# Performance work log

Measured on AMD Instinct MI355X. Metric: run time of the kernel, lower is better.

## Reference

```python
import jax, jax.numpy as jnp
import numpy as np

N_EMBD = 1024
N_HEAD = 16
HEAD_SIZE = 64
EPS = 1e-5


def _layer_norm(x, gamma, beta, eps=EPS):
    mu = jnp.mean(x, axis=-1, keepdims=True)
    var = jnp.mean(jnp.square(x - mu), axis=-1, keepdims=True)
    return (x - mu) * jax.lax.rsqrt(var + eps) * gamma + beta


def setup_inputs() -> dict:
    key = jax.random.key(0)
    ks = jax.random.split(key, 10)
    C = N_EMBD
    s = 1.0 / np.sqrt(C)
    x = jax.random.normal(ks[0], (4, 2048, C), dtype=jnp.float32)
    Wq = jax.random.normal(ks[1], (C, C), dtype=jnp.float32) * s
    Wk = jax.random.normal(ks[2], (C, C), dtype=jnp.float32) * s
    Wv = jax.random.normal(ks[3], (C, C), dtype=jnp.float32) * s
    Wo = jax.random.normal(ks[4], (C, C), dtype=jnp.float32) * s
    W1 = jax.random.normal(ks[5], (C, 4 * C), dtype=jnp.float32) * s
    b1 = jnp.zeros((4 * C,), dtype=jnp.float32)
    W2 = jax.random.normal(ks[6], (4 * C, C), dtype=jnp.float32) * (1.0 / np.sqrt(4 * C))
    b2 = jnp.zeros((C,), dtype=jnp.float32)
    g1 = jnp.ones((C,), dtype=jnp.float32)
    be1 = jnp.zeros((C,), dtype=jnp.float32)
    g2 = jnp.ones((C,), dtype=jnp.float32)
    be2 = jnp.zeros((C,), dtype=jnp.float32)
    return {"x": x, "Wq": Wq, "Wk": Wk, "Wv": Wv, "Wo": Wo,
            "W1": W1, "b1": b1, "W2": W2, "b2": b2,
            "g1": g1, "be1": be1, "g2": g2, "be2": be2}


def _block(x, Wq, Wk, Wv, Wo, W1, b1, W2, b2, g1, be1, g2, be2):
    B, T, C = x.shape
    H, D = N_HEAD, HEAD_SIZE
    # attention sub-block
    h = _layer_norm(x, g1, be1)
    q = (h @ Wq.T).reshape(B, T, H, D).transpose(0, 2, 1, 3)  # [B,H,T,D]
    k = (h @ Wk.T).reshape(B, T, H, D).transpose(0, 2, 1, 3)
    v = (h @ Wv.T).reshape(B, T, H, D).transpose(0, 2, 1, 3)
    wei = jnp.einsum("bhqd,bhkd->bhqk", q, k) * (D ** -0.5)
    causal = jnp.tril(jnp.ones((T, T), dtype=bool))
    wei = jnp.where(causal, wei, -jnp.inf)
    wei = jax.nn.softmax(wei, axis=-1)
    out = jnp.einsum("bhqk,bhkd->bhqd", wei, v)
    out = out.transpose(0, 2, 1, 3).reshape(B, T, C)
    x = x + out @ Wo.T
    # FFN sub-block (exact erf GELU, matching torch default)
    h2 = _layer_norm(x, g2, be2)
    ff = jax.nn.gelu(h2 @ W1 + b1, approximate=False) @ W2 + b2
    return x + ff


def reference(x, Wq, Wk, Wv, Wo, W1, b1, W2, b2, g1, be1, g2, be2):
    return _block(x, Wq, Wk, Wv, Wo, W1, b1, W2, b2, g1, be1, g2, be2)
```

## Files before the change

### kernel.cpp

```cpp
#include <hip/hip_runtime.h>
#include <cmath>

typedef unsigned short u16;
typedef __attribute__((ext_vector_type(8))) short bf16x8;
typedef __attribute__((ext_vector_type(4))) float f32x4;

#define TT 2048
#define CC 1024
#define BT 8192

__device__ __forceinline__ u16 f2bf(float f) {
  unsigned u = __builtin_bit_cast(unsigned, f);
  u += 0x7fffu + ((u >> 16) & 1u);
  return (u16)(u >> 16);
}

__device__ __forceinline__ void gload_lds16(const void* g, void* l) {
  __builtin_amdgcn_global_load_lds(
      (const __attribute__((address_space(1))) void*)g,
      (__attribute__((address_space(3))) void*)l, 16, 0, 0);
}


__global__ __launch_bounds__(256) void cvt_kernel(const float* __restrict__ s,
                                                  u16* __restrict__ d) {
  int i = (blockIdx.x * 256 + threadIdx.x) * 4;
  float4 v = *(const float4*)(s + i);
  ushort4 o;
  o.x = f2bf(v.x); o.y = f2bf(v.y); o.z = f2bf(v.z); o.w = f2bf(v.w);
  *(ushort4*)(d + i) = o;
}

__global__ __launch_bounds__(256) void transpose_cvt(const float* __restrict__ src,
                                                     u16* __restrict__ dst,
                                                     int R, int C) {
  __shared__ float tile[32][33];
  int c0 = blockIdx.x * 32, r0 = blockIdx.y * 32;
  int tx = threadIdx.x, ty = threadIdx.y;
#pragma unroll
  for (int j = 0; j < 4; ++j)
    tile[ty + j * 8][tx] = src[(size_t)(r0 + ty + j * 8) * C + c0 + tx];
  __syncthreads();
#pragma unroll
  for (int j = 0; j < 4; ++j)
    dst[(size_t)(c0 + ty + j * 8) * R + r0 + tx] = f2bf(tile[tx][ty + j * 8]);
}


__global__ __launch_bounds__(256) void ln_kernel(const float* __restrict__ x,
                                                 const float* __restrict__ gw,
                                                 const float* __restrict__ bw,
                                                 u16* __restrict__ out) {
  int row = blockIdx.x;
  int tid = threadIdx.x;
  const size_t base = (size_t)row * CC;
  float4 v = *(const float4*)(x + base + tid * 4);
  float s = v.x + v.y + v.z + v.w;
  float q = v.x * v.x + v.y * v.y + v.z * v.z + v.w * v.w;
#pragma unroll
  for (int o = 32; o > 0; o >>= 1) {
    s += __shfl_down(s, o, 64);
    q += __shfl_down(q, o, 64);
  }
  __shared__ float red[8];
  __shared__ float stat[2];
  int lane = tid & 63, wid = tid >> 6;
  if (!lane) { red[wid] = s; red[4 + wid] = q; }
  __syncthreads();
  if (!tid) {
    float S = red[0] + red[1] + red[2] + red[3];
    float Q = red[4] + red[5] + red[6] + red[7];
    float mu = S * (1.0f / CC);
    float var = Q * (1.0f / CC) - mu * mu;
    stat[0] = mu;
    stat[1] = rsqrtf(var + 1e-5f);
  }
  __syncthreads();
  float mu = stat[0], rs = stat[1];
  int c = tid * 4;
  float4 gv = *(const float4*)(gw + c);
  float4 bv = *(const float4*)(bw + c);
  ushort4 o;
  o.x = f2bf((v.x - mu) * rs * gv.x + bv.x);
  o.y = f2bf((v.y - mu) * rs * gv.y + bv.y);
  o.z = f2bf((v.z - mu) * rs * gv.z + bv.z);
  o.w = f2bf((v.w - mu) * rs * gv.w + bv.w);
  *(ushort4*)(out + base + c) = o;
}


template <int EPI>
__global__ __launch_bounds__(256) void gemm_bt(const u16* __restrict__ A,
                                               const u16* __restrict__ B,
                                               void* __restrict__ Cv,
                                               const float* __restrict__ bias,
                                               const float* __restrict__ resid,
                                               u16* __restrict__ vt,
                                               int N, int K) {
  __shared__ u16 As[4096];
  __shared__ u16 Bs[4096];
  const int tid = threadIdx.x, lane = tid & 63, wid = tid >> 6;
  const int tM = blockIdx.x * 128, tN = blockIdx.y * 128;
  const int wr = wid >> 1, wc = wid & 1;
  const int lr = lane >> 2, lc = (lane & 3) * 8;
  const int fr = lane & 15, fo = (lane >> 4) * 8;
  f32x4 acc[4][4] = {};
  const u16* Ab = A + (size_t)tM * K;
  const u16* Bb = B + (size_t)tN * K;
  for (int k0 = 0; k0 < K; k0 += 32) {
#pragma unroll
    for (int i = 0; i < 2; ++i) {
      int seg = wid * 2 + i;
      int row = seg * 16 + lr;
      gload_lds16(Ab + (size_t)row * K + k0 + lc, &As[seg * 512]);
      gload_lds16(Bb + (size_t)row * K + k0 + lc, &Bs[seg * 512]);
    }
    __syncthreads();
    bf16x8 af[4], bfr[4];
#pragma unroll
    for (int mi = 0; mi < 4; ++mi)
      af[mi] = *(const bf16x8*)&As[(wr * 64 + mi * 16 + fr) * 32 + fo];
#pragma unroll
    for (int ni = 0; ni < 4; ++ni)
      bfr[ni] = *(const bf16x8*)&Bs[(wc * 64 + ni * 16 + fr) * 32 + fo];
#pragma unroll
    for (int mi = 0; mi < 4; ++mi)
#pragma unroll
      for (int ni = 0; ni < 4; ++ni)
        acc[mi][ni] = __builtin_amdgcn_mfma_f32_16x16x32_bf16(af[mi], bfr[ni],
                                                              acc[mi][ni], 0, 0, 0);
    __syncthreads();
  }
  const int fq = lane >> 4;
#pragma unroll
  for (int mi = 0; mi < 4; ++mi) {
#pragma unroll
    for (int ni = 0; ni < 4; ++ni) {
      const int gR0 = tM + wr * 64 + mi * 16 + fq * 4;
      const int gC = tN + wc * 64 + ni * 16 + fr;
      if constexpr (EPI == 4) {
        if (gC < 2048) {
          float sc = (gC < 1024) ? 0.125f : 1.0f;
#pragma unroll
          for (int r = 0; r < 4; ++r)
            ((u16*)Cv)[(size_t)(gR0 + r) * 3072 + gC] = f2bf(acc[mi][ni][r] * sc);
        } else {
          int t = gR0 & 2047, bb = gR0 >> 11;
          int dv = gC - 2048, hh = dv >> 6, dd = dv & 63;
          int k5 = t & 31;
          int pos = ((k5 & 15) >> 2) * 8 + ((k5 >> 4) & 1) * 4;
          ushort4 q4;
          q4.x = f2bf(acc[mi][ni][0]);
          q4.y = f2bf(acc[mi][ni][1]);
          q4.z = f2bf(acc[mi][ni][2]);
          q4.w = f2bf(acc[mi][ni][3]);
          *(ushort4*)&vt[((size_t)((bb * 16 + hh) * 64 + dd)) * 2048 + (t & ~31) + pos] = q4;
        }
      } else {
#pragma unroll
        for (int r = 0; r < 4; ++r) {
          size_t idx = (size_t)(gR0 + r) * N + gC;
          float v = acc[mi][ni][r];
          if constexpr (EPI == 0) {
            ((u16*)Cv)[idx] = f2bf(v);
          } else if constexpr (EPI == 1) {
            ((float*)Cv)[idx] = v + resid[idx];
          } else if constexpr (EPI == 2) {
            v += bias[gC];
            v = 0.5f * v * (1.0f + erff(v * 0.70710678118f));
            ((u16*)Cv)[idx] = f2bf(v);
          } else {
            ((float*)Cv)[idx] = v + bias[gC] + resid[idx];
          }
        }
      }
    }
  }
}


__global__ __launch_bounds__(256) void attn_kernel(const u16* __restrict__ qkv,
                                                   const u16* __restrict__ vt,
                                                   u16* __restrict__ out) {
  const int pair = blockIdx.x;
  const int bh = blockIdx.y;
  const int b = bh >> 4, h = bh & 15;
  const int tid = threadIdx.x, lane = tid & 63, wid = tid >> 6;
  const int ql = lane & 15, g = lane >> 4;
  const int sw = ql & 7;
  __shared__ u16 Ks[2][4096];
  __shared__ u16 Vs[2][4096];
  const size_t rowQbase = (size_t)b * TT;
  const u16* kpart = qkv + rowQbase * 3072 + 1024 + h * 64;
  const u16* vpart = vt + ((size_t)(b * 16 + h) * 64) * 2048;
  const int srow = lane >> 3;
  const int sc16 = lane & 7;

  for (int pass = 0; pass < 2; ++pass) {
    const int qt = pass ? (31 - pair) : pair;
    const int qrow0 = qt * 64 + wid * 16;
    const int q_glb = qrow0 + ql;
    const u16* qp = qkv + (rowQbase + q_glb) * 3072 + h * 64 + g * 8;
    bf16x8 qf0 = *(const bf16x8*)qp;
    bf16x8 qf1 = *(const bf16x8*)(qp + 32);
    f32x4 o[4] = {};
    float m_run = -1e30f, l_run = 0.f;
    const int nt = qt + 1;

    auto stage = [&](int bufi, int t) {
      int kv0 = t * 64;
#pragma unroll
      for (int i = 0; i < 2; ++i) {
        int seg = wid * 2 + i;
        int rloc = seg * 8 + srow;
        int cs = (sc16 ^ (rloc & 7)) * 8;
        gload_lds16(kpart + (size_t)(kv0 + rloc) * 3072 + cs, &Ks[bufi][seg * 512]);
        gload_lds16(vpart + (size_t)rloc * 2048 + kv0 + cs, &Vs[bufi][seg * 512]);
      }
    };

    stage(0, 0);
    __syncthreads();
    int buf = 0;
    for (int t = 0; t < nt; ++t) {
      if (t + 1 < nt) stage(buf ^ 1, t + 1);
      const u16* Kb = Ks[buf];
      const u16* Vb = Vs[buf];
      const int kv0 = t * 64;
      float p[16];
#pragma unroll
      for (int kt = 0; kt < 4; ++kt) {
        int row = kt * 16 + ql;
        bf16x8 k0 = *(const bf16x8*)&Kb[row * 64 + ((g ^ sw) * 8)];
        bf16x8 k1 = *(const bf16x8*)&Kb[row * 64 + (((4 + g) ^ sw) * 8)];
        f32x4 s = {0.f, 0.f, 0.f, 0.f};
        s = __builtin_amdgcn_mfma_f32_16x16x32_bf16(k0, qf0, s, 0, 0, 0);
        s = __builtin_amdgcn_mfma_f32_16x16x32_bf16(k1, qf1, s, 0, 0, 0);
        if (t == qt) {
#pragma unroll
          for (int r = 0; r < 4; ++r) {
            int k_glb = kv0 + kt * 16 + 4 * g + r;
            p[kt * 4 + r] = (k_glb <= q_glb) ? s[r] : -1e30f;
          }
        } else {
#pragma unroll
          for (int r = 0; r < 4; ++r) p[kt * 4 + r] = s[r];
        }
      }
      float mloc = p[0];
#pragma unroll
      for (int i = 1; i < 16; ++i) mloc = fmaxf(mloc, p[i]);
      mloc = fmaxf(mloc, __shfl_xor(mloc, 16));
      mloc = fmaxf(mloc, __shfl_xor(mloc, 32));
      float mnew = fmaxf(m_run, mloc);
      float alpha = __expf(m_run - mnew);
      float lloc = 0.f;
      bf16x8 pa0, pa1;
#pragma unroll
      for (int i = 0; i < 16; ++i) {
        float e = __expf(p[i] - mnew);
        lloc += e;
        if (i < 8) pa0[i] = (short)f2bf(e);
        else pa1[i - 8] = (short)f2bf(e);
      }
      lloc += __shfl_xor(lloc, 16);
      lloc += __shfl_xor(lloc, 32);
      l_run = l_run * alpha + lloc;
      m_run = mnew;
      float aO[4];
#pragma unroll
      for (int r = 0; r < 4; ++r) aO[r] = __shfl(alpha, 4 * g + r);
#pragma unroll
      for (int d0 = 0; d0 < 4; ++d0) {
#pragma unroll
        for (int r = 0; r < 4; ++r) o[d0][r] *= aO[r];
      }
#pragma unroll
      for (int d0 = 0; d0 < 4; ++d0) {
        int row = d0 * 16 + ql;
        bf16x8 v0 = *(const bf16x8*)&Vb[row * 64 + ((g ^ sw) * 8)];
        bf16x8 v1 = *(const bf16x8*)&Vb[row * 64 + (((4 + g) ^ sw) * 8)];
        o[d0] = __builtin_amdgcn_mfma_f32_16x16x32_bf16(pa0, v0, o[d0], 0, 0, 0);
        o[d0] = __builtin_amdgcn_mfma_f32_16x16x32_bf16(pa1, v1, o[d0], 0, 0, 0);
      }
      __syncthreads();
      buf ^= 1;
    }
    float linv = 1.0f / l_run;
    float lO[4];
#pragma unroll
    for (int r = 0; r < 4; ++r) lO[r] = __shfl(linv, 4 * g + r);
#pragma unroll
    for (int d0 = 0; d0 < 4; ++d0) {
#pragma unroll
      for (int r = 0; r < 4; ++r) {
        size_t idx = (rowQbase + qrow0 + 4 * g + r) * CC + h * 64 + d0 * 16 + ql;
        out[idx] = f2bf(o[d0][r] * lO[r]);
      }
    }
  }
}


extern "C" void kernel_launch(void* const* d_in, const int* in_sizes, int n_in,
                              void* d_out, int out_size, void* d_ws, size_t ws_size,
                              hipStream_t stream) {
  const float* x   = (const float*)d_in[0];
  const float* Wq  = (const float*)d_in[1];
  const float* Wk  = (const float*)d_in[2];
  const float* Wv  = (const float*)d_in[3];
  const float* Wo  = (const float*)d_in[4];
  const float* W1  = (const float*)d_in[5];
  const float* b1  = (const float*)d_in[6];
  const float* W2  = (const float*)d_in[7];
  const float* b2  = (const float*)d_in[8];
  const float* g1  = (const float*)d_in[9];
  const float* be1 = (const float*)d_in[10];
  const float* g2  = (const float*)d_in[11];
  const float* be2 = (const float*)d_in[12];

  char* ws = (char*)d_ws;
  size_t off = 0;
  u16* Wqkv = (u16*)(ws + off); off += (size_t)3072 * 1024 * 2;
  u16* Wob  = (u16*)(ws + off); off += (size_t)1024 * 1024 * 2;
  u16* W1T  = (u16*)(ws + off); off += (size_t)4096 * 1024 * 2;
  u16* W2T  = (u16*)(ws + off); off += (size_t)1024 * 4096 * 2;
  u16* Hb   = (u16*)(ws + off); off += (size_t)BT * 1024 * 2;
  u16* QKV  = (u16*)(ws + off); off += (size_t)BT * 3072 * 2;
  u16* AttO = (u16*)(ws + off); off += (size_t)BT * 1024 * 2;
  float* X2 = (float*)(ws + off); off += (size_t)BT * 1024 * 4;
  u16* FF1 = QKV;
  u16* VT  = (u16*)X2;
  if (ws_size < off) return;

  cvt_kernel<<<1024, 256, 0, stream>>>(Wq, Wqkv);
  cvt_kernel<<<1024, 256, 0, stream>>>(Wk, Wqkv + 1024 * 1024);
  cvt_kernel<<<1024, 256, 0, stream>>>(Wv, Wqkv + 2 * 1024 * 1024);
  cvt_kernel<<<1024, 256, 0, stream>>>(Wo, Wob);
  transpose_cvt<<<dim3(128, 32), dim3(32, 8), 0, stream>>>(W1, W1T, 1024, 4096);
  transpose_cvt<<<dim3(32, 128), dim3(32, 8), 0, stream>>>(W2, W2T, 4096, 1024);

  ln_kernel<<<BT, 256, 0, stream>>>(x, g1, be1, Hb);
  gemm_bt<4><<<dim3(64, 24), 256, 0, stream>>>(Hb, Wqkv, QKV, nullptr, nullptr, VT, 3072, 1024);
  attn_kernel<<<dim3(16, 64), 256, 0, stream>>>(QKV, VT, AttO);
  gemm_bt<1><<<dim3(64, 8), 256, 0, stream>>>(AttO, Wob, X2, nullptr, x, nullptr, 1024, 1024);
  ln_kernel<<<BT, 256, 0, stream>>>(X2, g2, be2, Hb);
  gemm_bt<2><<<dim3(64, 32), 256, 0, stream>>>(Hb, W1T, FF1, b1, nullptr, nullptr, 4096, 1024);
  gemm_bt<3><<<dim3(64, 8), 256, 0, stream>>>(FF1, W2T, (float*)d_out, b2, X2, nullptr, 1024, 4096);
}
```

Measured before the change: 460.9 us.

## Add 256x256-tile pipelined GEMM for QKV and FFN1 projections

```diff
diff --git a/kernel.cpp b/kernel.cpp
--- a/kernel.cpp
+++ b/kernel.cpp
@@ -138,40 +138,133 @@
     for (int ni = 0; ni < 4; ++ni) {
       const int gR0 = tM + wr * 64 + mi * 16 + fq * 4;
       const int gC = tN + wc * 64 + ni * 16 + fr;
+#pragma unroll
+      for (int r = 0; r < 4; ++r) {
+        size_t idx = (size_t)(gR0 + r) * N + gC;
+        float v = acc[mi][ni][r];
+        if constexpr (EPI == 1) {
+          ((float*)Cv)[idx] = v + resid[idx];
+        } else {
+          ((float*)Cv)[idx] = v + bias[gC] + resid[idx];
+        }
+      }
+    }
+  }
+}
+
+
+template <int EPI>
+__global__ __launch_bounds__(512) void gemm256(const u16* __restrict__ A,
+                                               const u16* __restrict__ B,
+                                               void* __restrict__ Cv,
+                                               const float* __restrict__ bias,
+                                               u16* __restrict__ vt,
+                                               int N, int K, int gn) {
+  __shared__ u16 lds[8][8192];
+  const int tid = threadIdx.x, lane = tid & 63, wid = tid >> 6;
+  const int nwg = gridDim.x;
+  const int bid = blockIdx.x;
+  const int sb = (nwg & 7) ? bid : ((bid & 7) * (nwg >> 3) + (bid >> 3));
+  const int tM = (sb / gn) * 256, tN = (sb % gn) * 256;
+  const int wm = wid >> 2, wn = wid & 3;
+  const int fr = lane & 15, g4 = lane >> 4;
+  const int gsw = (g4 ^ ((fr >> 3) << 1)) * 8;
+  const int srow0 = wid * 16 + (lane >> 2);
+  const int scol = ((lane & 3) ^ ((lane >> 5) << 1)) * 8;
+  const u16* Ab = A + (size_t)tM * K;
+  const u16* Bb = B + (size_t)tN * K;
+  const int NKT = K >> 6;
+  f32x4 acc[8][4] = {};
+
+  auto stage = [&](int idx) {
+    int ts = idx >> 2, h = idx & 3;
+    const u16* G = (h & 1) ? Bb : Ab;
+    size_t kof = (size_t)ts * 64 + (h >> 1) * 32;
+    u16* dst = lds[idx & 7];
+#pragma unroll
+    for (int i = 0; i < 2; ++i)
+      gload_lds16(G + (size_t)(srow0 + i * 128) * K + kof + scol,
+                  dst + (size_t)(i * 512 + wid * 64) * 8);
+  };
+
+#pragma unroll
+  for (int j = 0; j < 4; ++j) stage(j);
+  asm volatile("s_waitcnt vmcnt(4)" ::: "memory");
+#pragma unroll
+  for (int j = 4; j < 7; ++j) stage(j);
+  asm volatile("s_waitcnt vmcnt(6)" ::: "memory");
+  __builtin_amdgcn_s_barrier();
+
+  for (int t = 0; t < NKT; ++t) {
+    const int bo = (t & 1) << 2;
+#pragma unroll
+    for (int ks = 0; ks < 2; ++ks) {
+      const u16* Ah = lds[bo | (ks << 1)];
+      const u16* Bh = lds[bo | (ks << 1) | 1];
+      bf16x8 bfr[4];
+#pragma unroll
+      for (int ni = 0; ni < 4; ++ni)
+        bfr[ni] = *(const bf16x8*)&Bh[(wn * 64 + ni * 16 + fr) * 32 + gsw];
+#pragma unroll
+      for (int mh = 0; mh < 2; ++mh) {
+        bf16x8 af[4];
+#pragma unroll
+        for (int mi = 0; mi < 4; ++mi)
+          af[mi] = *(const bf16x8*)&Ah[(wm * 128 + mh * 64 + mi * 16 + fr) * 32 + gsw];
+        __builtin_amdgcn_sched_barrier(0);
+        int idx = 4 * t + (ks << 1) + mh + 7;
+        if (idx < 4 * NKT) stage(idx);
+        __builtin_amdgcn_s_barrier();
+        asm volatile("s_waitcnt lgkmcnt(0)" ::: "memory");
+        __builtin_amdgcn_sched_barrier(0);
+        __builtin_amdgcn_s_setprio(1);
+#pragma unroll
+        for (int mi = 0; mi < 4; ++mi)
+#pragma unroll
+          for (int ni = 0; ni < 4; ++ni)
+            acc[mh * 4 + mi][ni] = __builtin_amdgcn_mfma_f32_16x16x32_bf16(
+                af[mi], bfr[ni], acc[mh * 4 + mi][ni], 0, 0, 0);
+        __builtin_amdgcn_s_setprio(0);
+        __builtin_amdgcn_sched_barrier(0);
+        if (ks == 1 && mh == 1) {
+          if (t < NKT - 2) asm volatile("s_waitcnt vmcnt(6)" ::: "memory");
+          else if (t == NKT - 2) asm volatile("s_waitcnt vmcnt(0)" ::: "memory");
+        }
+        __builtin_amdgcn_s_barrier();
+      }
+    }
+  }
+
+#pragma unroll
+  for (int m = 0; m < 8; ++m) {
+#pragma unroll
+    for (int ni = 0; ni < 4; ++ni) {
+      const int gR0 = tM + wm * 128 + m * 16 + g4 * 4;
+      const int gC = tN + wn * 64 + ni * 16 + fr;
       if constexpr (EPI == 4) {
         if (gC < 2048) {
           float sc = (gC < 1024) ? 0.125f : 1.0f;
 #pragma unroll
           for (int r = 0; r < 4; ++r)
-            ((u16*)Cv)[(size_t)(gR0 + r) * 3072 + gC] = f2bf(acc[mi][ni][r] * sc);
+            ((u16*)Cv)[(size_t)(gR0 + r) * 3072 + gC] = f2bf(acc[m][ni][r] * sc);
         } else {
-          int t = gR0 & 2047, bb = gR0 >> 11;
+          int tr = gR0 & 2047, bb = gR0 >> 11;
           int dv = gC - 2048, hh = dv >> 6, dd = dv & 63;
-          int k5 = t & 31;
+          int k5 = tr & 31;
           int pos = ((k5 & 15) >> 2) * 8 + ((k5 >> 4) & 1) * 4;
           ushort4 q4;
-          q4.x = f2bf(acc[mi][ni][0]);
-          q4.y = f2bf(acc[mi][ni][1]);
-          q4.z = f2bf(acc[mi][ni][2]);
-          q4.w = f2bf(acc[mi][ni][3]);
-          *(ushort4*)&vt[((size_t)((bb * 16 + hh) * 64 + dd)) * 2048 + (t & ~31) + pos] = q4;
+          q4.x = f2bf(acc[m][ni][0]);
+          q4.y = f2bf(acc[m][ni][1]);
+          q4.z = f2bf(acc[m][ni][2]);
+          q4.w = f2bf(acc[m][ni][3]);
+          *(ushort4*)&vt[((size_t)((bb * 16 + hh) * 64 + dd)) * 2048 + (tr & ~31) + pos] = q4;
         }
       } else {
 #pragma unroll
         for (int r = 0; r < 4; ++r) {
-          size_t idx = (size_t)(gR0 + r) * N + gC;
-          float v = acc[mi][ni][r];
-          if constexpr (EPI == 0) {
-            ((u16*)Cv)[idx] = f2bf(v);
-          } else if constexpr (EPI == 1) {
-            ((float*)Cv)[idx] = v + resid[idx];
-          } else if constexpr (EPI == 2) {
-            v += bias[gC];
-            v = 0.5f * v * (1.0f + erff(v * 0.70710678118f));
-            ((u16*)Cv)[idx] = f2bf(v);
-          } else {
-            ((float*)Cv)[idx] = v + bias[gC] + resid[idx];
-          }
+          float v = acc[m][ni][r] + bias[gC];
+          v = 0.5f * v * (1.0f + erff(v * 0.70710678118f));
+          ((u16*)Cv)[(size_t)(gR0 + r) * N + gC] = f2bf(v);
         }
       }
     }
@@ -341,10 +434,10 @@
   transpose_cvt<<<dim3(32, 128), dim3(32, 8), 0, stream>>>(W2, W2T, 4096, 1024);
 
   ln_kernel<<<BT, 256, 0, stream>>>(x, g1, be1, Hb);
-  gemm_bt<4><<<dim3(64, 24), 256, 0, stream>>>(Hb, Wqkv, QKV, nullptr, nullptr, VT, 3072, 1024);
+  gemm256<4><<<32 * 12, 512, 0, stream>>>(Hb, Wqkv, QKV, nullptr, VT, 3072, 1024, 12);
   attn_kernel<<<dim3(16, 64), 256, 0, stream>>>(QKV, VT, AttO);
   gemm_bt<1><<<dim3(64, 8), 256, 0, stream>>>(AttO, Wob, X2, nullptr, x, nullptr, 1024, 1024);
   ln_kernel<<<BT, 256, 0, stream>>>(X2, g2, be2, Hb);
-  gemm_bt<2><<<dim3(64, 32), 256, 0, stream>>>(Hb, W1T, FF1, b1, nullptr, nullptr, 4096, 1024);
+  gemm256<2><<<32 * 16, 512, 0, stream>>>(Hb, W1T, FF1, b1, nullptr, 4096, 1024, 16);
   gemm_bt<3><<<dim3(64, 8), 256, 0, stream>>>(FF1, W2T, (float*)d_out, b2, X2, nullptr, 1024, 4096);
 }
```

Result: no change. 455.8 us (-1.1%).
